# Kernel tuning notes

Hardware: AMD Instinct MI355X
Metric: run time of the kernel (lower is better)

## Reference

```python
import jax, jax.numpy as jnp
import numpy as np

KH, KW = 3, 3  # spatial kernel from kernel_size=(1,3,3,C)


def _extract_patches_valid(x, kh, kw):
    # TF extract_image_patches ordering: depth = (row, col, channel) flattened.
    B, H, W, C = x.shape
    Ho, Wo = H - kh + 1, W - kw + 1
    # stack kh*kw shifted views -> [B, Ho, Wo, kh*kw, C]
    views = [x[:, i:i + Ho, j:j + Wo, :] for i in range(kh) for j in range(kw)]
    patches = jnp.stack(views, axis=3)
    return patches.reshape(B, Ho, Wo, kh * kw * C)


def setup_inputs() -> dict:
    key = jax.random.key(0)
    k1, k2, k3 = jax.random.split(key, 3)
    B, H, W, C = 32, 112, 112, 32
    filters = 128
    patch_dim = KH * KW * C  # 288
    x = jax.random.normal(k1, (B, H, W, C), dtype=jnp.float32)
    ccs = jax.random.uniform(k2, (patch_dim, filters), dtype=jnp.float32)  # RandomUniform(0,1)
    beta = jax.random.uniform(k3, (filters,), dtype=jnp.float32)
    return {"x": x, "ccs": ccs, "beta": beta}


def reference(x, ccs, beta):
    B = x.shape[0]
    patch_dim, filters = ccs.shape
    patches = _extract_patches_valid(x, KH, KW)  # [B, Ho, Wo, patch_dim]
    Ho, Wo = patches.shape[1], patches.shape[2]
    p = patches.reshape(B, Ho * Wo, patch_dim)  # [B, P, D]
    # squared distance: ||p||^2 - 2 p.ccs + ||ccs||^2  -> [B, P, filters]
    p_sq = jnp.sum(p * p, axis=2, keepdims=True)
    c_sq = jnp.sum(ccs * ccs, axis=0, keepdims=True)
    scores = p_sq - 2.0 * jnp.einsum('bpd,df->bpf', p, ccs) + c_sq
    out = jnp.exp(-beta * scores)  # RBF activation, beta broadcast over filters
    return out.reshape(B, Ho, Wo, filters)
```

## Files before the change

kernel.cpp:

```cpp
#include <hip/hip_runtime.h>


typedef __attribute__((ext_vector_type(8))) short bf16x8;
typedef __attribute__((ext_vector_type(4))) float f32x4;

#define HH 112
#define WW 112
#define CC 32
#define HO 110
#define WO 110
#define NF 128
#define KD 288
#define XPITCH 40

__device__ __forceinline__ unsigned short f32_to_bf16(float f) {
    unsigned u = __float_as_uint(f);
    unsigned r = u + 0x7FFFu + ((u >> 16) & 1u);
    return (unsigned short)(r >> 16);
}

__global__ __launch_bounds__(256) void rbf_prologue(const float* __restrict__ ccs,
                                                    unsigned short* __restrict__ ccs_t,
                                                    float* __restrict__ c_sq) {
    int idx = blockIdx.x * 256 + threadIdx.x;
    int d = idx >> 7;
    int f = idx & 127;
    float v = ccs[idx];
    ccs_t[f * KD + d] = f32_to_bf16(v);
    atomicAdd(&c_sq[f], v * v);
}

__global__ __launch_bounds__(256) void rbf_main(const float* __restrict__ x,
                                                const unsigned short* __restrict__ ccs_t,
                                                const float* __restrict__ c_sq,
                                                const float* __restrict__ beta,
                                                float* __restrict__ out) {
    __shared__ unsigned short xs[3 * 130 * XPITCH];
    __shared__ float colsum[3 * 112 + 8];
    __shared__ float p_sq[128];

    const int t = threadIdx.x;
    const int y = blockIdx.x;
    const int b = blockIdx.y;

    const float* xrow = x + (size_t)((b * HH + y) * WW) * CC;

    #pragma unroll
    for (int p = 0; p < 11; ++p) {
        int idx = t + p * 256;
        if (idx < 2688) {
            int q = idx & 7;
            int ic = idx >> 3;
            int col = ic % 112;
            int i = ic / 112;
            const float4 v = *(const float4*)(xrow + (i * WW + col) * CC + q * 4);
            unsigned short h0 = f32_to_bf16(v.x), h1 = f32_to_bf16(v.y);
            unsigned short h2 = f32_to_bf16(v.z), h3 = f32_to_bf16(v.w);
            uint2 pk;
            pk.x = (unsigned)h0 | ((unsigned)h1 << 16);
            pk.y = (unsigned)h2 | ((unsigned)h3 << 16);
            *(uint2*)(&xs[(i * 130 + col) * XPITCH + q * 4]) = pk;
            float part = v.x * v.x + v.y * v.y + v.z * v.z + v.w * v.w;
            part += __shfl_xor(part, 1);
            part += __shfl_xor(part, 2);
            part += __shfl_xor(part, 4);
            if (q == 0) colsum[ic] = part;
        }
    }
    __syncthreads();

    if (t < 112) {
        float s = 0.f;
        #pragma unroll
        for (int i = 0; i < 3; ++i)
            #pragma unroll
            for (int j = 0; j < 3; ++j)
                s += colsum[i * 112 + t + j];
        p_sq[t] = s;
    }
    __syncthreads();

    const int lane  = t & 63;
    const int wave  = t >> 6;
    const int laneM = lane & 15;
    const int quad  = lane >> 4;

    const int n0 = wave * 32 + laneM;
    const int n1 = n0 + 16;
    const float csq0 = c_sq[n0], csq1 = c_sq[n1];
    const float bt0  = beta[n0], bt1  = beta[n1];

    f32x4 acc[7][2];
    #pragma unroll
    for (int mi = 0; mi < 7; ++mi) {
        acc[mi][0] = (f32x4){0.f, 0.f, 0.f, 0.f};
        acc[mi][1] = (f32x4){0.f, 0.f, 0.f, 0.f};
    }

    const unsigned short* bp0 = ccs_t + n0 * KD + quad * 8;
    const unsigned short* bp1 = ccs_t + n1 * KD + quad * 8;

    #pragma unroll
    for (int kb = 0; kb < 9; ++kb) {
        const int ki = kb / 3, kj = kb % 3;
        bf16x8 b0 = *(const bf16x8*)(bp0 + kb * 32);
        bf16x8 b1 = *(const bf16x8*)(bp1 + kb * 32);
        #pragma unroll
        for (int mi = 0; mi < 7; ++mi) {
            const bf16x8 a = *(const bf16x8*)(&xs[(ki * 130 + mi * 16 + laneM + kj) * XPITCH + quad * 8]);
            acc[mi][0] = __builtin_amdgcn_mfma_f32_16x16x32_bf16(a, b0, acc[mi][0], 0, 0, 0);
            acc[mi][1] = __builtin_amdgcn_mfma_f32_16x16x32_bf16(a, b1, acc[mi][1], 0, 0, 0);
        }
    }

    float* orow = out + (size_t)((b * HO + y) * WO) * NF;
    #pragma unroll
    for (int mi = 0; mi < 7; ++mi) {
        #pragma unroll
        for (int r = 0; r < 4; ++r) {
            int m = mi * 16 + quad * 4 + r;
            if (m < WO) {
                float ps = p_sq[m];
                float s0 = ps - 2.f * acc[mi][0][r] + csq0;
                float s1 = ps - 2.f * acc[mi][1][r] + csq1;
                orow[(size_t)m * NF + n0] = __expf(-bt0 * s0);
                orow[(size_t)m * NF + n1] = __expf(-bt1 * s1);
            }
        }
    }
}

extern "C" void kernel_launch(void* const* d_in, const int* in_sizes, int n_in,
                              void* d_out, int out_size, void* d_ws, size_t ws_size,
                              hipStream_t stream) {
    const float* x    = (const float*)d_in[0];
    const float* ccs  = (const float*)d_in[1];
    const float* beta = (const float*)d_in[2];
    float* out = (float*)d_out;

    unsigned short* ccs_t = (unsigned short*)d_ws;
    float* c_sq = (float*)((char*)d_ws + 128 * KD * sizeof(unsigned short));

    hipMemsetAsync(c_sq, 0, NF * sizeof(float), stream);
    rbf_prologue<<<144, 256, 0, stream>>>(ccs, ccs_t, c_sq);
    rbf_main<<<dim3(HO, 32), 256, 0, stream>>>(x, ccs_t, c_sq, beta, out);
}
```

Before: 284.2 us.

## Swap MFMA operands for vectorized float4 stores and compute two rows per block

Transposes the MFMA operand roles so each lane holds four consecutive filters, letting the RBF output be written as float4 instead of scattered scalars. Each block now processes two output rows, loading four input rows into shared memory and reusing the middle rows across both. This cuts redundant input loads and improves store coalescing. The cost is halving the grid and adding more LDS per block, which may reduce occupancy.

```diff
diff --git a/kernel.cpp b/kernel.cpp
--- a/kernel.cpp
+++ b/kernel.cpp
@@ -11,7 +11,8 @@
 #define WO 110
 #define NF 128
 #define KD 288
-#define XPITCH 40
+#define RPX 114
+#define XP 40
 
 __device__ __forceinline__ unsigned short f32_to_bf16(float f) {
     unsigned u = __float_as_uint(f);
@@ -35,47 +36,47 @@
                                                 const float* __restrict__ c_sq,
                                                 const float* __restrict__ beta,
                                                 float* __restrict__ out) {
-    __shared__ unsigned short xs[3 * 130 * XPITCH];
-    __shared__ float colsum[3 * 112 + 8];
-    __shared__ float p_sq[128];
+    __shared__ unsigned short xs[4 * RPX * XP];
+    __shared__ float colsum[456];
+    __shared__ float p_sq[2 * 112];
 
     const int t = threadIdx.x;
-    const int y = blockIdx.x;
+    const int y0 = blockIdx.x * 2;
     const int b = blockIdx.y;
 
-    const float* xrow = x + (size_t)((b * HH + y) * WW) * CC;
+    const float* xbase = x + (size_t)((b * HH + y0) * WW) * CC;
 
     #pragma unroll
-    for (int p = 0; p < 11; ++p) {
+    for (int p = 0; p < 14; ++p) {
         int idx = t + p * 256;
-        if (idx < 2688) {
-            int q = idx & 7;
-            int ic = idx >> 3;
-            int col = ic % 112;
-            int i = ic / 112;
-            const float4 v = *(const float4*)(xrow + (i * WW + col) * CC + q * 4);
-            unsigned short h0 = f32_to_bf16(v.x), h1 = f32_to_bf16(v.y);
-            unsigned short h2 = f32_to_bf16(v.z), h3 = f32_to_bf16(v.w);
-            uint2 pk;
-            pk.x = (unsigned)h0 | ((unsigned)h1 << 16);
-            pk.y = (unsigned)h2 | ((unsigned)h3 << 16);
-            *(uint2*)(&xs[(i * 130 + col) * XPITCH + q * 4]) = pk;
-            float part = v.x * v.x + v.y * v.y + v.z * v.z + v.w * v.w;
-            part += __shfl_xor(part, 1);
-            part += __shfl_xor(part, 2);
-            part += __shfl_xor(part, 4);
-            if (q == 0) colsum[ic] = part;
-        }
+        int q = idx & 7;
+        int ic = idx >> 3;
+        int col = ic % 112;
+        int i = ic / 112;
+        const float4 v = *(const float4*)(xbase + (i * WW + col) * CC + q * 4);
+        unsigned short h0 = f32_to_bf16(v.x), h1 = f32_to_bf16(v.y);
+        unsigned short h2 = f32_to_bf16(v.z), h3 = f32_to_bf16(v.w);
+        uint2 pk;
+        pk.x = (unsigned)h0 | ((unsigned)h1 << 16);
+        pk.y = (unsigned)h2 | ((unsigned)h3 << 16);
+        *(uint2*)(&xs[(i * RPX + col) * XP + q * 4]) = pk;
+        float part = v.x * v.x + v.y * v.y + v.z * v.z + v.w * v.w;
+        part += __shfl_xor(part, 1);
+        part += __shfl_xor(part, 2);
+        part += __shfl_xor(part, 4);
+        if (q == 0) colsum[ic] = part;
     }
     __syncthreads();
 
-    if (t < 112) {
+    if (t < 224) {
+        int r = (t >= 112) ? 1 : 0;
+        int c = t - r * 112;
         float s = 0.f;
         #pragma unroll
         for (int i = 0; i < 3; ++i)
             #pragma unroll
             for (int j = 0; j < 3; ++j)
-                s += colsum[i * 112 + t + j];
+                s += colsum[(r + i) * 112 + c + j];
         p_sq[t] = s;
     }
     __syncthreads();
@@ -85,46 +86,54 @@
     const int laneM = lane & 15;
     const int quad  = lane >> 4;
 
-    const int n0 = wave * 32 + laneM;
-    const int n1 = n0 + 16;
-    const float csq0 = c_sq[n0], csq1 = c_sq[n1];
-    const float bt0  = beta[n0], bt1  = beta[n1];
+    const unsigned short* ap0 = ccs_t + (size_t)(wave * 32 + laneM) * KD + quad * 8;
+    const unsigned short* ap1 = ap0 + 16 * KD;
 
-    f32x4 acc[7][2];
-    #pragma unroll
-    for (int mi = 0; mi < 7; ++mi) {
-        acc[mi][0] = (f32x4){0.f, 0.f, 0.f, 0.f};
-        acc[mi][1] = (f32x4){0.f, 0.f, 0.f, 0.f};
-    }
-
-    const unsigned short* bp0 = ccs_t + n0 * KD + quad * 8;
-    const unsigned short* bp1 = ccs_t + n1 * KD + quad * 8;
+    const int fb = wave * 32 + quad * 4;
+    const float4 cs0 = *(const float4*)(c_sq + fb);
+    const float4 cs1 = *(const float4*)(c_sq + fb + 16);
+    const float4 bt0 = *(const float4*)(beta + fb);
+    const float4 bt1 = *(const float4*)(beta + fb + 16);
 
     #pragma unroll
-    for (int kb = 0; kb < 9; ++kb) {
-        const int ki = kb / 3, kj = kb % 3;
-        bf16x8 b0 = *(const bf16x8*)(bp0 + kb * 32);
-        bf16x8 b1 = *(const bf16x8*)(bp1 + kb * 32);
+    for (int r = 0; r < 2; ++r) {
+        f32x4 acc[7][2];
         #pragma unroll
         for (int mi = 0; mi < 7; ++mi) {
-            const bf16x8 a = *(const bf16x8*)(&xs[(ki * 130 + mi * 16 + laneM + kj) * XPITCH + quad * 8]);
-            acc[mi][0] = __builtin_amdgcn_mfma_f32_16x16x32_bf16(a, b0, acc[mi][0], 0, 0, 0);
-            acc[mi][1] = __builtin_amdgcn_mfma_f32_16x16x32_bf16(a, b1, acc[mi][1], 0, 0, 0);
+            acc[mi][0] = (f32x4){0.f, 0.f, 0.f, 0.f};
+            acc[mi][1] = (f32x4){0.f, 0.f, 0.f, 0.f};
         }
-    }
 
-    float* orow = out + (size_t)((b * HO + y) * WO) * NF;
-    #pragma unroll
-    for (int mi = 0; mi < 7; ++mi) {
         #pragma unroll
-        for (int r = 0; r < 4; ++r) {
-            int m = mi * 16 + quad * 4 + r;
-            if (m < WO) {
-                float ps = p_sq[m];
-                float s0 = ps - 2.f * acc[mi][0][r] + csq0;
-                float s1 = ps - 2.f * acc[mi][1][r] + csq1;
-                orow[(size_t)m * NF + n0] = __expf(-bt0 * s0);
-                orow[(size_t)m * NF + n1] = __expf(-bt1 * s1);
+        for (int kb = 0; kb < 9; ++kb) {
+            const int ki = kb / 3, kj = kb % 3;
+            bf16x8 a0 = *(const bf16x8*)(ap0 + kb * 32);
+            bf16x8 a1 = *(const bf16x8*)(ap1 + kb * 32);
+            #pragma unroll
+            for (int mi = 0; mi < 7; ++mi) {
+                const bf16x8 bf = *(const bf16x8*)(&xs[((r + ki) * RPX + mi * 16 + laneM + kj) * XP + quad * 8]);
+                acc[mi][0] = __builtin_amdgcn_mfma_f32_16x16x32_bf16(a0, bf, acc[mi][0], 0, 0, 0);
+                acc[mi][1] = __builtin_amdgcn_mfma_f32_16x16x32_bf16(a1, bf, acc[mi][1], 0, 0, 0);
+            }
+        }
+
+        float* orow = out + (size_t)((b * HO + y0 + r) * WO) * NF;
+        #pragma unroll
+        for (int mi = 0; mi < 7; ++mi) {
+            const int px = mi * 16 + laneM;
+            const float ps = p_sq[r * 112 + px];
+            float* op = orow + (size_t)px * NF + fb;
+            #pragma unroll
+            for (int ft = 0; ft < 2; ++ft) {
+                const float4 cs = ft ? cs1 : cs0;
+                const float4 bt = ft ? bt1 : bt0;
+                float4 o;
+                o.x = __expf(-bt.x * (ps - 2.f * acc[mi][ft][0] + cs.x));
+                o.y = __expf(-bt.y * (ps - 2.f * acc[mi][ft][1] + cs.y));
+                o.z = __expf(-bt.z * (ps - 2.f * acc[mi][ft][2] + cs.z));
+                o.w = __expf(-bt.w * (ps - 2.f * acc[mi][ft][3] + cs.w));
+                if (px < WO)
+                    *(float4*)(op + ft * 16) = o;
             }
         }
     }
@@ -143,5 +152,5 @@
 
     hipMemsetAsync(c_sq, 0, NF * sizeof(float), stream);
     rbf_prologue<<<144, 256, 0, stream>>>(ccs, ccs_t, c_sq);
-    rbf_main<<<dim3(HO, 32), 256, 0, stream>>>(x, ccs_t, c_sq, beta, out);
+    rbf_main<<<dim3(55, 32), 256, 0, stream>>>(x, ccs_t, c_sq, beta, out);
 }
```

Result: no change. 287.4 us (+1.1%).
